# Kernel tuning notes

Hardware: AMD Instinct MI355X
Metric: run time of the kernel (lower is better)

## Reference

```python
import jax, jax.numpy as jnp
import numpy as np

PROB_THR = 0.05
NMS_THR = 0.45
VAR0, VAR1 = 0.1, 0.2
TOP_K = 100


def setup_inputs() -> dict:
    key = jax.random.key(0)
    k1, k2, k3, k4 = jax.random.split(key, 4)
    N, A, C = 8, 16384, 21
    classifications = jax.random.normal(k1, (N, A, C), jnp.float32)
    regressions = jax.random.normal(k2, (N, A, 4), jnp.float32) * 0.5
    centers = jax.random.uniform(k3, (A, 2), dtype=jnp.float32)            # anchor centers in [0,1]
    wh = jax.random.uniform(k4, (A, 2), dtype=jnp.float32, minval=0.02, maxval=0.3)  # anchor sizes
    anchors = jnp.concatenate([centers, wh], axis=-1)                      # [A,4] (cx,cy,w,h)
    return {"classifications": classifications, "regressions": regressions, "anchors": anchors}


def _decode_to_corners(loc, anchors):
    # SSD decode: loc [N,A,4], anchors [A,4] (cx,cy,w,h) -> clamped corner boxes [N,A,4]
    cxcy = anchors[:, :2] + loc[..., :2] * VAR0 * anchors[:, 2:]
    wh = anchors[:, 2:] * jnp.exp(loc[..., 2:] * VAR1)
    half = wh * 0.5
    corners = jnp.concatenate([cxcy - half, cxcy + half], axis=-1)
    return jnp.clip(corners, 0.0, 1.0)


def _forward(classifications, regressions, anchors):
    N, A, C = classifications.shape
    sft = jax.nn.softmax(classifications, axis=-1)                 # [N,A,C]
    boxes = _decode_to_corners(regressions, anchors)               # [N,A,4]
    area_all = (boxes[..., 2] - boxes[..., 0]) * (boxes[..., 3] - boxes[..., 1])  # [N,A]

    # per-class scores, background (class 0) excluded; below-threshold -> -1 (inactive)
    scores0 = jnp.swapaxes(sft[..., 1:], 1, 2)                     # [N,C-1,A]
    scores0 = jnp.where(scores0 > PROB_THR, scores0, -1.0)
    cls_ids = jnp.arange(1, C, dtype=classifications.dtype)        # [C-1]
    batch_ix = jnp.arange(N)[:, None]
    anchor_ix = jnp.arange(A)

    def step(scores, _):
        # scores: [N,C-1,A]
        idx = jnp.argmax(scores, axis=-1)                          # [N,C-1]
        best = jnp.take_along_axis(scores, idx[..., None], axis=-1)[..., 0]
        valid = best > 0.0
        sel = boxes[batch_ix, idx]                                 # [N,C-1,4]
        # IoU of selected box against all boxes of the image: [N,C-1,A]
        lt = jnp.maximum(sel[..., None, :2], boxes[:, None, :, :2])
        rb = jnp.minimum(sel[..., None, 2:], boxes[:, None, :, 2:])
        whi = jnp.clip(rb - lt, 0.0)
        inter = whi[..., 0] * whi[..., 1]
        area_sel = (sel[..., 2] - sel[..., 0]) * (sel[..., 3] - sel[..., 1])
        union = area_sel[..., None] + area_all[:, None, :] - inter
        iou = jnp.where(union > 0.0, inter / union, 0.0)
        self_mask = anchor_ix[None, None, :] == idx[..., None]
        kill = valid[..., None] & ((iou > NMS_THR) | self_mask)
        new_scores = jnp.where(kill, -1.0, scores)
        cls_col = jnp.broadcast_to(cls_ids[None, :, None], best[..., None].shape)
        row = jnp.concatenate([sel, best[..., None], cls_col], axis=-1)    # [N,C-1,6]
        row = jnp.where(valid[..., None], row, 0.0)
        return new_scores, row

    _, rows = jax.lax.scan(jax.checkpoint(step), scores0, None, length=TOP_K)
    rows = jnp.transpose(rows, (1, 2, 0, 3))                       # [N,C-1,TOP_K,6]
    full = jnp.concatenate(
        [jnp.zeros((N, 1, TOP_K, 6), rows.dtype), rows], axis=1
    ).reshape(N, C * TOP_K, 6)                                     # class 0 row kept as zeros
    scores_col = full[..., 4]
    _, top_idx = jax.lax.top_k(scores_col, TOP_K)                  # [N,TOP_K]
    top = jnp.take_along_axis(full, top_idx[..., None], axis=1)    # [N,TOP_K,6]
    return top


def reference(classifications, regressions, anchors):
    return _forward(classifications, regressions, anchors)
```

## Files before the change

kernel.cpp:

```cpp
#include <hip/hip_runtime.h>


typedef unsigned long long u64;

#define N_IMG 8
#define A     16384
#define NCLS  21
#define NC    20
#define TOPK  100
#define PROB_THR 0.05f

#define TN     512
#define NSLOT  32
#define NBIN   1152
#define BINOFF 31385
#define CAPC   512
#define TARGET 384

#define PHYS(i) ((i) + ((i) >> 4))

#define MIDTHR ((double)0.45f + 0x1p-26)

#define AIDX(t_) ((tid << 2) + (((t_) >> 2) << 11) + ((t_) & 3))

__device__ __forceinline__ u64 pk(float v, int i) {
    return (v > 0.f) ? (((u64)__float_as_uint(v) << 32) | (u64)(unsigned)(~(unsigned)i)) : 0ull;
}
__device__ __forceinline__ float upv(u64 k) { return __uint_as_float((unsigned)(k >> 32)); }
__device__ __forceinline__ int   upi(u64 k) { return (int)(~(unsigned)k); }
__device__ __forceinline__ u64 umx(u64 a, u64 b) { return a > b ? a : b; }
__device__ __forceinline__ u64 umn(u64 a, u64 b) { return a < b ? a : b; }

__device__ __forceinline__ u64 bsel(u64 mine, u64 other, int i, int k, int j) {
    bool keep_max = ((i & k) == 0) == ((i & j) == 0);
    return keep_max ? umx(mine, other) : umn(mine, other);
}

__device__ __forceinline__ int binOf(float s) {
    int b = (int)(__float_as_uint(s) >> 15) - BINOFF;
    return b < 0 ? 0 : (b > NBIN - 1 ? NBIN - 1 : b);
}

__device__ __forceinline__ bool killp(float4 b, float ab, float4 s, float as_) {
    float lx = fmaxf(s.x, b.x), ly = fmaxf(s.y, b.y);
    float rx = fminf(s.z, b.z), ry = fminf(s.w, b.w);
    float iw = fmaxf(rx - lx, 0.f), ih = fmaxf(ry - ly, 0.f);
    float inter = iw * ih;
    float un = as_ + ab - inter;
    return (double)inter > MIDTHR * (double)un;
}

__global__ __launch_bounds__(256) void preprocess_kernel(
    const float* __restrict__ cls, const float* __restrict__ reg,
    const float* __restrict__ anc, float4* __restrict__ boxes,
    float* __restrict__ scores) {
    __shared__ __align__(16) float lcls[256 * NCLS];
    const int tid = threadIdx.x;
    const int t = blockIdx.x * 256 + tid;

    const float4* src = (const float4*)(cls + (size_t)blockIdx.x * (256 * NCLS));
    float4* dst = (float4*)lcls;
    for (int i = tid; i < (256 * NCLS) / 4; i += 256) dst[i] = src[i];
    __syncthreads();

    const int n = t >> 14;
    const int a = t & (A - 1);
    const float* c = lcls + tid * NCLS;
    float z[NCLS];
    float m = -1e30f;
#pragma unroll
    for (int k = 0; k < NCLS; ++k) { z[k] = c[k]; m = fmaxf(m, z[k]); }
    float s = 0.f;
#pragma unroll
    for (int k = 0; k < NCLS; ++k) { z[k] = expf(z[k] - m); s += z[k]; }
    const float inv = 1.f / s;
#pragma unroll
    for (int k = 0; k < NC; ++k) {
        float p = z[k + 1] * inv;
        scores[(((size_t)n * NC + k) << 14) + a] = (p > PROB_THR) ? p : -1.f;
    }

    const float4 l4 = ((const float4*)reg)[t];
    const float4 an = ((const float4*)anc)[a];
    const float cx = an.x + l4.x * 0.1f * an.z;
    const float cy = an.y + l4.y * 0.1f * an.w;
    const float w  = an.z * expf(l4.z * 0.2f);
    const float h  = an.w * expf(l4.w * 0.2f);
    float x0 = fminf(fmaxf(cx - 0.5f * w, 0.f), 1.f);
    float y0 = fminf(fmaxf(cy - 0.5f * h, 0.f), 1.f);
    float x1 = fminf(fmaxf(cx + 0.5f * w, 0.f), 1.f);
    float y1 = fminf(fmaxf(cy + 0.5f * h, 0.f), 1.f);
    boxes[t] = make_float4(x0, y0, x1, y1);
}

__global__ __launch_bounds__(TN) void nms_kernel(
    const float4* __restrict__ boxes, const float* __restrict__ scores,
    float* __restrict__ rows) {
    __shared__ int bins[NBIN];
    __shared__ u64 skey[PHYS(CAPC - 1) + 2];
    __shared__ __align__(16) float4 sbox[CAPC];
    __shared__ float sarea[CAPC];
    __shared__ u64 gm[8][64];
    __shared__ u64 dm[8];
    __shared__ __align__(16) float4 abox[TOPK];
    __shared__ float aarea[TOPK];
    __shared__ u64 akey[TOPK];
    __shared__ u64 red8[TN / 64];
    __shared__ u64 bkey;
    __shared__ __align__(16) float4 bbox;
    __shared__ int sint[3];

    const int blk = blockIdx.x, n = blk / NC, ci = blk % NC;
    const int tid = threadIdx.x, lane = tid & 63, w = tid >> 6;
    const float* gs = scores + ((size_t)blk << 14);
    const float4* gb = boxes + ((size_t)n << 14);
    float* grows = rows + (size_t)blk * 600;

    float sc[NSLOT];
    const float4* gs4 = (const float4*)gs;
#pragma unroll
    for (int k = 0; k < NSLOT / 4; ++k) {
        float4 v = gs4[tid + (k << 9)];
        sc[k * 4 + 0] = v.x; sc[k * 4 + 1] = v.y; sc[k * 4 + 2] = v.z; sc[k * 4 + 3] = v.w;
    }

    int na = 0;
    u64 filter = ~0ull;
    bool done = false;

    while (!done && na < TOPK) {
        for (int i = tid; i < NBIN; i += TN) bins[i] = 0;
        if (tid == 0) { sint[1] = 0; sint[2] = 0; }
        __syncthreads();
#pragma unroll
        for (int t = 0; t < NSLOT; ++t) {
            float s = sc[t];
            if (s > 0.f) {
                u64 kk = pk(s, AIDX(t));
                if (kk < filter) atomicAdd(&bins[binOf(s)], 1);
            }
        }
        __syncthreads();

        if (tid < 64) {
            int lsum[18];
            int tot = 0;
#pragma unroll
            for (int k = 0; k < 18; ++k) { lsum[k] = bins[tid * 18 + k]; tot += lsum[k]; }
            int pfx = tot;
#pragma unroll
            for (int off = 1; off < 64; off <<= 1) {
                int o = __shfl_up(pfx, off, 64);
                if (lane >= off) pfx += o;
            }
            const int totalAll = __shfl(pfx, 63, 64);
            const int sufAbove = totalAll - pfx;
            const int tgt = totalAll < TARGET ? totalAll : TARGET;
            int run = 0, b1 = -1, b2 = 1 << 30;
#pragma unroll
            for (int k = 17; k >= 0; --k) {
                run += lsum[k];
                int suf = sufAbove + run;
                int b = tid * 18 + k;
                if (suf >= tgt && b > b1) b1 = b;
                if (suf <= CAPC && b < b2) b2 = b;
            }
#pragma unroll
            for (int off = 1; off < 64; off <<= 1) {
                int o1 = __shfl_xor(b1, off, 64); if (o1 > b1) b1 = o1;
                int o2 = __shfl_xor(b2, off, 64); if (o2 < b2) b2 = o2;
            }
            if (lane == 0) {
                sint[0] = b1 > b2 ? b1 : b2;
                sint[2] = (b2 == (1 << 30)) ? 1 : 0;
            }
        }
        __syncthreads();
        const int B = sint[0];
        const int degen = sint[2];

        if (!degen) {
#pragma unroll
            for (int t = 0; t < NSLOT; ++t) {
                float s = sc[t];
                bool pred = false; u64 kk = 0ull;
                if (s > 0.f && binOf(s) >= B) {
                    kk = pk(s, AIDX(t));
                    pred = (kk < filter);
                }
                u64 m = __ballot(pred);
                if (m) {
                    int bse = 0;
                    if (lane == 0) bse = atomicAdd(&sint[1], __popcll(m));
                    bse = __shfl(bse, 0, 64);
                    if (pred) {
                        int sl = bse + __popcll(m & ((1ull << lane) - 1ull));
                        skey[PHYS(sl)] = kk;
                    }
                }
            }
            __syncthreads();
            const int T = sint[1];
            if (T == 0) break;
            for (int i = T + tid; i < CAPC; i += TN) skey[PHYS(i)] = 0ull;
            __syncthreads();

            {
                u64 myk = skey[PHYS(tid)];
                for (int kk2 = 2; kk2 <= CAPC; kk2 <<= 1) {
                    for (int j = kk2 >> 1; j > 0; j >>= 1) {
                        u64 other;
                        if (j >= 64) {
                            skey[PHYS(tid)] = myk;
                            __syncthreads();
                            other = skey[PHYS(tid ^ j)];
                            __syncthreads();
                        } else {
                            other = __shfl_xor(myk, j, 64);
                        }
                        myk = bsel(myk, other, tid, kk2, j);
                    }
                }
                skey[PHYS(tid)] = myk;
            }
            __syncthreads();

            for (int p = tid; p < CAPC; p += TN) {
                u64 kk = skey[PHYS(p)];
                if (kk) {
                    float4 b = gb[upi(kk)];
                    sbox[p] = b;
                    sarea[p] = (b.z - b.x) * (b.w - b.y);
                }
            }
            __syncthreads();

            for (int base = 0; base < T && na < TOPK; base += 64) {
                const int cnt = (T - base < 64) ? (T - base) : 64;
                const float4 cb = sbox[base + lane];
                const float ca = sarea[base + lane];
                __syncthreads();

                bool d = false;
                for (int q = w; q < na; q += 8)
                    d = d || killp(cb, ca, abox[q], aarea[q]);
                u64 dball = __ballot(d);
                if (lane == 0) dm[w] = dball;

                u64 pr = 0ull;
#pragma unroll
                for (int e = 0; e < 8; ++e) {
                    const int jj = (w << 3) + e;
                    bool kp = (jj < lane) && killp(cb, ca, sbox[base + jj], sarea[base + jj]);
                    pr |= ((u64)kp) << jj;
                }
                gm[w][lane] = pr;
                __syncthreads();

                u64 row = gm[0][lane];
#pragma unroll
                for (int q = 1; q < 8; ++q) row |= gm[q][lane];
                u64 dead = dm[0];
#pragma unroll
                for (int q = 1; q < 8; ++q) dead |= dm[q];

                u64 alive = ~dead;
                if (cnt < 64) alive &= (1ull << cnt) - 1ull;
                u64 gacc = 0ull;
                int naL = na;
                while (alive && naL < TOPK) {
                    const int g = (int)__builtin_ctzll(alive);
                    gacc |= 1ull << g;
                    ++naL;
                    const u64 colg = __ballot(((row >> g) & 1ull) != 0ull);
                    alive &= ~colg;
                    alive &= ~(1ull << g);
                }

                if (w == 0 && ((gacc >> lane) & 1ull)) {
                    const int pos = na + (int)__popcll(gacc & ((1ull << lane) - 1ull));
                    abox[pos] = cb;
                    aarea[pos] = ca;
                    akey[pos] = skey[PHYS(base + lane)];
                }
                na = naL;
            }
            done = (na >= TOPK);
            if (!done) filter = skey[PHYS(T - 1)];
            __syncthreads();
        } else {
            while (na < TOPK) {
                u64 best = 0ull;
#pragma unroll
                for (int t = 0; t < NSLOT; ++t) {
                    float s = sc[t];
                    if (s > 0.f) {
                        u64 kk = pk(s, AIDX(t));
                        if (kk < filter && kk > best) best = kk;
                    }
                }
#pragma unroll
                for (int off = 1; off < 64; off <<= 1) best = umx(best, __shfl_xor(best, off, 64));
                if (lane == 0) red8[w] = best;
                __syncthreads();
                if (tid == 0) {
                    u64 bb = red8[0];
#pragma unroll
                    for (int q = 1; q < TN / 64; ++q) bb = umx(bb, red8[q]);
                    bkey = bb;
                    if (bb) bbox = gb[upi(bb)];
                }
                __syncthreads();
                u64 kk = bkey;
                if (!kk) break;
                filter = kk;
                float4 cb = bbox;
                float ca = (cb.z - cb.x) * (cb.w - cb.y);
                bool kill = false;
                if (lane < na)      kill = killp(cb, ca, abox[lane], aarea[lane]);
                if (lane + 64 < na) kill = kill || killp(cb, ca, abox[lane + 64], aarea[lane + 64]);
                if (!__any(kill)) {
                    if (tid == 0) { abox[na] = cb; aarea[na] = ca; akey[na] = kk; }
                    ++na;
                }
                __syncthreads();
            }
            break;
        }
    }

    __syncthreads();
    if (tid < na) {
        float4 b = abox[tid];
        u64 kk = akey[tid];
        float* o = grows + tid * 6;
        o[0] = b.x; o[1] = b.y; o[2] = b.z; o[3] = b.w;
        o[4] = upv(kk); o[5] = (float)(ci + 1);
    }
    for (int j = na * 6 + tid; j < 600; j += TN) grows[j] = 0.f;
}

__global__ __launch_bounds__(1024) void topk_kernel(
    const float* __restrict__ rows, float* __restrict__ out) {
    __shared__ u64 skey[PHYS(2047) + 2];
    const int n = blockIdx.x, tid = threadIdx.x;
    const float* base = rows + (size_t)n * (NC * 600);
    const int i0 = tid << 1, i1 = i0 | 1;

    u64 k0 = 0ull, k1 = 0ull;
    if (i0 < 2000) {
        int ci = i0 / 100, pos = i0 - ci * 100;
        float s = base[ci * 600 + pos * 6 + 4];
        k0 = ((u64)__float_as_uint(s) << 32) | (u64)(0xFFFFFFFFu - (unsigned)(i0 + 100));
    }
    if (i1 < 2000) {
        int ci = i1 / 100, pos = i1 - ci * 100;
        float s = base[ci * 600 + pos * 6 + 4];
        k1 = ((u64)__float_as_uint(s) << 32) | (u64)(0xFFFFFFFFu - (unsigned)(i1 + 100));
    }

    for (int kk2 = 2; kk2 <= 2048; kk2 <<= 1) {
        for (int j = kk2 >> 1; j > 0; j >>= 1) {
            if (j >= 128) {
                skey[PHYS(i0)] = k0; skey[PHYS(i1)] = k1;
                __syncthreads();
                u64 o0 = skey[PHYS(i0 ^ j)], o1 = skey[PHYS(i1 ^ j)];
                __syncthreads();
                k0 = bsel(k0, o0, i0, kk2, j);
                k1 = bsel(k1, o1, i1, kk2, j);
            } else if (j >= 2) {
                u64 o0 = __shfl_xor(k0, j >> 1, 64);
                u64 o1 = __shfl_xor(k1, j >> 1, 64);
                k0 = bsel(k0, o0, i0, kk2, j);
                k1 = bsel(k1, o1, i1, kk2, j);
            } else {
                bool mx0 = ((i0 & kk2) == 0);
                u64 mx = umx(k0, k1), mn = umn(k0, k1);
                k0 = mx0 ? mx : mn; k1 = mx0 ? mn : mx;
            }
        }
    }
    skey[PHYS(i0)] = k0; skey[PHYS(i1)] = k1;
    __syncthreads();

    if (tid < 600) {
        int r = tid / 6, f = tid - (tid / 6) * 6;
        u64 kk = skey[PHYS(r)];
        float v = 0.f;
        if ((unsigned)(kk >> 32) != 0u) {
            int e = (int)(0xFFFFFFFFu - (unsigned)kk) - 100;
            int ci = e / 100, pos = e - ci * 100;
            v = base[ci * 600 + pos * 6 + f];
        }
        out[(size_t)n * 600 + tid] = v;
    }
}

extern "C" void kernel_launch(void* const* d_in, const int* in_sizes, int n_in,
                              void* d_out, int out_size, void* d_ws, size_t ws_size,
                              hipStream_t stream) {
    const float* cls = (const float*)d_in[0];
    const float* reg = (const float*)d_in[1];
    const float* anc = (const float*)d_in[2];
    float* out = (float*)d_out;

    float* boxes  = (float*)d_ws;
    float* scores = boxes + (size_t)N_IMG * A * 4;
    float* rows   = scores + (size_t)N_IMG * NC * A;

    preprocess_kernel<<<(N_IMG * A) / 256, 256, 0, stream>>>(cls, reg, anc, (float4*)boxes, scores);
    nms_kernel<<<N_IMG * NC, TN, 0, stream>>>((const float4*)boxes, scores, rows);
    topk_kernel<<<N_IMG, 1024, 0, stream>>>(rows, out);
}
```

Baseline: 114.3 us.

## Privatize histogram bins per wave pair and size bitonic sort to candidate count

Splits the shared score histogram into four copies, one per pair of waves, so atomic contention during binning drops; the copies are summed during the prefix scan. The bitonic sort now runs only over the next power of two at or above the candidate count instead of always 512, skipping stages and shared-memory barriers when fewer candidates survive. TARGET is raised from 384 to 448 so each round gathers more candidates, which may cut the number of rounds but makes each sort larger. The change costs extra shared memory and a wider zeroing loop each round.

```diff
diff --git a/kernel.cpp b/kernel.cpp
--- a/kernel.cpp
+++ b/kernel.cpp
@@ -15,7 +15,7 @@
 #define NBIN   1152
 #define BINOFF 31385
 #define CAPC   512
-#define TARGET 384
+#define TARGET 448
 
 #define PHYS(i) ((i) + ((i) >> 4))
 
@@ -96,7 +96,7 @@
 __global__ __launch_bounds__(TN) void nms_kernel(
     const float4* __restrict__ boxes, const float* __restrict__ scores,
     float* __restrict__ rows) {
-    __shared__ int bins[NBIN];
+    __shared__ int bins4[4][NBIN];
     __shared__ u64 skey[PHYS(CAPC - 1) + 2];
     __shared__ __align__(16) float4 sbox[CAPC];
     __shared__ float sarea[CAPC];
@@ -129,15 +129,16 @@
     bool done = false;
 
     while (!done && na < TOPK) {
-        for (int i = tid; i < NBIN; i += TN) bins[i] = 0;
+        for (int i = tid; i < 4 * NBIN; i += TN) ((int*)bins4)[i] = 0;
         if (tid == 0) { sint[1] = 0; sint[2] = 0; }
         __syncthreads();
+        int* mybins = bins4[w >> 1];
 #pragma unroll
         for (int t = 0; t < NSLOT; ++t) {
             float s = sc[t];
             if (s > 0.f) {
                 u64 kk = pk(s, AIDX(t));
-                if (kk < filter) atomicAdd(&bins[binOf(s)], 1);
+                if (kk < filter) atomicAdd(&mybins[binOf(s)], 1);
             }
         }
         __syncthreads();
@@ -146,7 +147,11 @@
             int lsum[18];
             int tot = 0;
 #pragma unroll
-            for (int k = 0; k < 18; ++k) { lsum[k] = bins[tid * 18 + k]; tot += lsum[k]; }
+            for (int k = 0; k < 18; ++k) {
+                int b = tid * 18 + k;
+                lsum[k] = bins4[0][b] + bins4[1][b] + bins4[2][b] + bins4[3][b];
+                tot += lsum[k];
+            }
             int pfx = tot;
 #pragma unroll
             for (int off = 1; off < 64; off <<= 1) {
@@ -202,30 +207,33 @@
             __syncthreads();
             const int T = sint[1];
             if (T == 0) break;
-            for (int i = T + tid; i < CAPC; i += TN) skey[PHYS(i)] = 0ull;
+            int S = 64;
+            while (S < T) S <<= 1;
+            for (int i = T + tid; i < S; i += TN) skey[PHYS(i)] = 0ull;
             __syncthreads();
 
             {
-                u64 myk = skey[PHYS(tid)];
-                for (int kk2 = 2; kk2 <= CAPC; kk2 <<= 1) {
+                const bool act = (tid < S);
+                u64 myk = act ? skey[PHYS(tid)] : 0ull;
+                for (int kk2 = 2; kk2 <= S; kk2 <<= 1) {
                     for (int j = kk2 >> 1; j > 0; j >>= 1) {
-                        u64 other;
                         if (j >= 64) {
-                            skey[PHYS(tid)] = myk;
+                            if (act) skey[PHYS(tid)] = myk;
                             __syncthreads();
-                            other = skey[PHYS(tid ^ j)];
+                            u64 other = act ? skey[PHYS(tid ^ j)] : 0ull;
                             __syncthreads();
+                            if (act) myk = bsel(myk, other, tid, kk2, j);
                         } else {
-                            other = __shfl_xor(myk, j, 64);
+                            u64 other = __shfl_xor(myk, j, 64);
+                            if (act) myk = bsel(myk, other, tid, kk2, j);
                         }
-                        myk = bsel(myk, other, tid, kk2, j);
                     }
                 }
-                skey[PHYS(tid)] = myk;
+                if (act) skey[PHYS(tid)] = myk;
             }
             __syncthreads();
 
-            for (int p = tid; p < CAPC; p += TN) {
+            for (int p = tid; p < S; p += TN) {
                 u64 kk = skey[PHYS(p)];
                 if (kk) {
                     float4 b = gb[upi(kk)];
```

New measurement: 118.3 us. 1.04x slower.
